# Kernel optimization log

Hardware: AMD Instinct MI355X
Metric: run time of the kernel (lower is better)

Reference implementation:

```python
import jax, jax.numpy as jnp
import numpy as np

N = 100000
E = 3200000
N_IN = 512
N_OUT = 256


def setup_inputs() -> dict:
    key = jax.random.key(0)
    k = jax.random.split(key, 6)
    stdv = 1.0 / np.sqrt(N_IN)
    x = jax.random.normal(k[0], (N, N_IN), dtype=jnp.float32)
    adj_rows = jax.random.randint(k[1], (E,), 0, N, dtype=jnp.int32)
    adj_cols = jax.random.randint(k[2], (E,), 0, N, dtype=jnp.int32)
    adj_vals = jax.random.uniform(k[3], (E,), dtype=jnp.float32)
    W = jax.random.uniform(k[4], (N_OUT, N_IN), minval=-stdv, maxval=stdv, dtype=jnp.float32)
    b = jax.random.uniform(k[5], (N_OUT,), minval=-stdv, maxval=stdv, dtype=jnp.float32)
    return {"x": x, "adj_rows": adj_rows, "adj_cols": adj_cols, "adj_vals": adj_vals, "W": W, "b": b}


def reference(x, adj_rows, adj_cols, adj_vals, W, b):
    # linear projection: x @ W^T + b  -> [N, n_out]
    h = jnp.einsum('ni,oi->no', x, W) + b
    # spmm: out[r] = sum_e adj_vals[e] * h[adj_cols[e]] for edges with row r
    msgs = h[adj_cols] * adj_vals[:, None]          # [E, n_out]
    out = jax.ops.segment_sum(msgs, adj_rows, num_segments=N)
    return out
```

## Files before the change

### kernel.cpp

```cpp
#include <hip/hip_runtime.h>

#define NIN 512
#define NOUT 256
#define NPART 8
#define RPB 32
#define BSH 5
#define CHUNK 2048
#define CSH 11
#define SEG 256
#define SEGSH 8
#define SCAT 1024

typedef __attribute__((ext_vector_type(8))) __bf16 bf16x8;
typedef __attribute__((ext_vector_type(4))) float f32x4;
typedef __attribute__((ext_vector_type(2))) int i32x2;

__device__ __forceinline__ ushort f2bf(float f) {
  uint u = __builtin_bit_cast(uint, f);
  uint r = (u + 0x7FFFu + ((u >> 16) & 1u)) >> 16;
  return (ushort)r;
}
__device__ __forceinline__ uint pk2(float a, float b) {
  return (uint)f2bf(a) | ((uint)f2bf(b) << 16);
}
__device__ __forceinline__ float bf2f(ushort u) {
  return __builtin_bit_cast(float, (uint)u << 16);
}

__global__ __launch_bounds__(256) void init_cur_kernel(int* __restrict__ cur,
                                                       int NB) {
  int i = blockIdx.x * 256 + threadIdx.x;
  if (i < NPART * NB) {
    int s = i / NB;
    int b = i - s * NB;
    cur[i] = ((b << 3) + s) << SEGSH;
  }
}

__global__ __launch_bounds__(512) void gemm_scatter_kernel(
    const float* __restrict__ x, const float* __restrict__ W,
    const float* __restrict__ bias, ushort* __restrict__ h, int M,
    const int* __restrict__ rows, const int* __restrict__ cols,
    const float* __restrict__ vals, int* __restrict__ cur,
    int2* __restrict__ bufE, int E, int NB, int nchunks, int G) {
  __shared__ ushort a_lds[128 * 40];
  __shared__ ushort b_lds[256 * 40];

  const int t = threadIdx.x;

  if (blockIdx.x >= G) {
    const int s = blockIdx.x & (NPART - 1);
    const int j = (int)blockIdx.x - G;
    const int m = j >> 3;
    const int nres = SCAT >> 3;
    int* mycur = cur + s * NB;
    for (int k = m;; k += nres) {
      int c = k * NPART + s;
      if (c >= nchunks) break;
      int i0 = c << CSH;
      int i1 = min(E, i0 + CHUNK);
      for (int i = i0 + t; i < i1; i += 512) {
        int r = __builtin_nontemporal_load(&rows[i]);
        int cc = __builtin_nontemporal_load(&cols[i]);
        float vv = __builtin_nontemporal_load(&vals[i]);
        int pos = atomicAdd(&mycur[r >> BSH], 1);
        int2 p;
        p.x = ((r & (RPB - 1)) << 17) | cc;
        p.y = __builtin_bit_cast(int, vv);
        bufE[pos] = p;
      }
    }
    return;
  }

  const int l = t & 63;
  const int wv = t >> 6;
  const int wr = wv >> 2;
  const int wc = wv & 3;
  const int m0 = blockIdx.x * 128;

  const int lrow = l & 15;
  const int lk = (l >> 4) * 8;

  f32x4 acc[4][4];
#pragma unroll
  for (int i = 0; i < 4; ++i)
#pragma unroll
    for (int j = 0; j < 4; ++j) acc[i][j] = (f32x4){0.f, 0.f, 0.f, 0.f};

  float biasr[4];
#pragma unroll
  for (int j = 0; j < 4; ++j) biasr[j] = bias[wc * 64 + j * 16 + lrow];

  const int arow = t >> 2;
  const int akc = (t & 3) * 8;
  const int brow = t >> 1;
  const int bkc = (t & 1) * 16;

  for (int k0 = 0; k0 < NIN; k0 += 32) {
    {
      float4 v0 = make_float4(0.f, 0.f, 0.f, 0.f), v1 = v0;
      if (m0 + arow < M) {
        const float4* xs =
            reinterpret_cast<const float4*>(x + (size_t)(m0 + arow) * NIN + k0 + akc);
        v0 = xs[0];
        v1 = xs[1];
      }
      uint4 p;
      p.x = pk2(v0.x, v0.y); p.y = pk2(v0.z, v0.w);
      p.z = pk2(v1.x, v1.y); p.w = pk2(v1.z, v1.w);
      *reinterpret_cast<uint4*>(&a_lds[arow * 40 + akc]) = p;
    }
    {
      const float4* wsrc =
          reinterpret_cast<const float4*>(W + (size_t)brow * NIN + k0 + bkc);
      float4 w0 = wsrc[0], w1 = wsrc[1], w2 = wsrc[2], w3 = wsrc[3];
      uint4 p0, p1;
      p0.x = pk2(w0.x, w0.y); p0.y = pk2(w0.z, w0.w);
      p0.z = pk2(w1.x, w1.y); p0.w = pk2(w1.z, w1.w);
      p1.x = pk2(w2.x, w2.y); p1.y = pk2(w2.z, w2.w);
      p1.z = pk2(w3.x, w3.y); p1.w = pk2(w3.z, w3.w);
      *reinterpret_cast<uint4*>(&b_lds[brow * 40 + bkc]) = p0;
      *reinterpret_cast<uint4*>(&b_lds[brow * 40 + bkc + 8]) = p1;
    }
    __syncthreads();

    bf16x8 af[4], bf_[4];
#pragma unroll
    for (int i = 0; i < 4; ++i)
      af[i] = *reinterpret_cast<const bf16x8*>(
          &a_lds[(wr * 64 + i * 16 + lrow) * 40 + lk]);
#pragma unroll
    for (int j = 0; j < 4; ++j)
      bf_[j] = *reinterpret_cast<const bf16x8*>(
          &b_lds[(wc * 64 + j * 16 + lrow) * 40 + lk]);
#pragma unroll
    for (int i = 0; i < 4; ++i)
#pragma unroll
      for (int j = 0; j < 4; ++j)
        acc[i][j] = __builtin_amdgcn_mfma_f32_16x16x32_bf16(af[i], bf_[j],
                                                            acc[i][j], 0, 0, 0);
    __syncthreads();
  }

#pragma unroll
  for (int i = 0; i < 4; ++i) {
    const int mbase = m0 + wr * 64 + i * 16 + (l >> 4) * 4;
#pragma unroll
    for (int r = 0; r < 4; ++r) {
      int m = mbase + r;
      if (m >= M) continue;
#pragma unroll
      for (int j = 0; j < 4; ++j)
        h[(size_t)m * NOUT + wc * 64 + j * 16 + lrow] =
            f2bf(acc[i][j][r] + biasr[j]);
    }
  }
}

__global__ __launch_bounds__(256) void bucket_reduce_kernel(
    const ushort* __restrict__ h, const int2* __restrict__ bufE,
    const int* __restrict__ cur, float* __restrict__ out, int M, int NB) {
  __shared__ int2 sbuf[NPART * SEG];
  __shared__ int cnt[RPB];
  __shared__ int off[RPB + 1];
  __shared__ int segn[NPART];

  const int b = blockIdx.x;
  const int t = threadIdx.x;

  if (t < NPART)
    segn[t] = min(cur[t * NB + b] - (((b << 3) + t) << SEGSH), SEG);
  if (t < RPB) cnt[t] = 0;
  __syncthreads();

  int2 ed[NPART];
#pragma unroll
  for (int s = 0; s < NPART; ++s) {
    int2 p = make_int2(0, 0);
    if (t < segn[s]) {
      i32x2 raw = __builtin_nontemporal_load(reinterpret_cast<const i32x2*>(
          &bufE[(size_t)(((b << 3) + s) << SEGSH) + t]));
      p.x = raw.x;
      p.y = raw.y;
      atomicAdd(&cnt[(uint)p.x >> 17], 1);
    }
    ed[s] = p;
  }
  __syncthreads();
  if (t == 0) {
    int run = 0;
#pragma unroll
    for (int j = 0; j < RPB; ++j) { off[j] = run; run += cnt[j]; }
    off[RPB] = run;
  }
  __syncthreads();
  if (t < RPB) cnt[t] = off[t];
  __syncthreads();
#pragma unroll
  for (int s = 0; s < NPART; ++s) {
    if (t < segn[s]) {
      int pos = atomicAdd(&cnt[(uint)ed[s].x >> 17], 1);
      sbuf[pos] = ed[s];
    }
  }
  __syncthreads();

  const int wv = t >> 6;
  const int lane = t & 63;
  for (int q = 0; q < 8; ++q) {
    int j = wv * 8 + q;
    int row = b * RPB + j;
    if (row >= M) break;
    int e = off[j];
    const int e1 = off[j + 1];
    f32x4 acc = (f32x4){0.f, 0.f, 0.f, 0.f};
    for (; e + 7 < e1; e += 8) {
      ushort4 hv[8];
      float vv[8];
#pragma unroll
      for (int u = 0; u < 8; ++u) {
        int2 p = sbuf[e + u];
        vv[u] = __builtin_bit_cast(float, p.y);
        hv[u] = *reinterpret_cast<const ushort4*>(
            h + (size_t)(p.x & 0x1FFFF) * NOUT + lane * 4);
      }
#pragma unroll
      for (int u = 0; u < 8; ++u) {
        acc.x += vv[u] * bf2f(hv[u].x);
        acc.y += vv[u] * bf2f(hv[u].y);
        acc.z += vv[u] * bf2f(hv[u].z);
        acc.w += vv[u] * bf2f(hv[u].w);
      }
    }
    for (; e < e1; ++e) {
      int2 p0 = sbuf[e];
      float v0 = __builtin_bit_cast(float, p0.y);
      ushort4 h0 = *reinterpret_cast<const ushort4*>(
          h + (size_t)(p0.x & 0x1FFFF) * NOUT + lane * 4);
      acc.x += v0 * bf2f(h0.x); acc.y += v0 * bf2f(h0.y);
      acc.z += v0 * bf2f(h0.z); acc.w += v0 * bf2f(h0.w);
    }
    __builtin_nontemporal_store(
        acc, reinterpret_cast<f32x4*>(out + (size_t)row * NOUT + lane * 4));
  }
}

extern "C" void kernel_launch(void* const* d_in, const int* in_sizes, int n_in,
                              void* d_out, int out_size, void* d_ws, size_t ws_size,
                              hipStream_t stream) {
  const float* x        = (const float*)d_in[0];
  const int*   adj_rows = (const int*)d_in[1];
  const int*   adj_cols = (const int*)d_in[2];
  const float* adj_vals = (const float*)d_in[3];
  const float* W        = (const float*)d_in[4];
  const float* b        = (const float*)d_in[5];
  float* out = (float*)d_out;

  const int M = in_sizes[0] / NIN;
  const int E = in_sizes[1];

  const int NB = (M + RPB - 1) >> BSH;
  const int nchunks = (E + CHUNK - 1) >> CSH;

  ushort* h    = (ushort*)d_ws;
  int2*   bufE = (int2*)(h + (size_t)M * NOUT);
  int*    cur  = (int*)(bufE + (size_t)NB * NPART * SEG);

  const int G = (M + 127) / 128;

  init_cur_kernel<<<(NPART * NB + 255) / 256, 256, 0, stream>>>(cur, NB);
  gemm_scatter_kernel<<<G + SCAT, 512, 0, stream>>>(
      x, W, b, h, M, adj_rows, adj_cols, adj_vals, cur, bufE, E, NB, nchunks, G);
  bucket_reduce_kernel<<<NB, 256, 0, stream>>>(h, bufE, cur, out, M, NB);
}
```

Before: 420.6 us.

## Split wavefront halves across edges with 16-byte gathers; prefetch next x tile in GEMM

The reduce kernel now has each half-wavefront handle a different edge, with each lane gathering 8 bf16 values (16 bytes) instead of 4. The two halves' partial sums are then combined with a shuffle before the store. This widens the per-lane gather and processes two edges per instruction, at the cost of extra shuffles and an odd-edge tail path. The GEMM also loads the next k-slice of x into registers before the MFMA work so global latency overlaps compute, at the cost of extra registers.

New measurement: 420.9 us. About the same (+0.1%).

```diff
diff --git a/kernel.cpp b/kernel.cpp
--- a/kernel.cpp
+++ b/kernel.cpp
@@ -13,7 +13,9 @@
 
 typedef __attribute__((ext_vector_type(8))) __bf16 bf16x8;
 typedef __attribute__((ext_vector_type(4))) float f32x4;
+typedef __attribute__((ext_vector_type(8))) float f32x8;
 typedef __attribute__((ext_vector_type(2))) int i32x2;
+typedef __attribute__((ext_vector_type(8))) ushort u16x8;
 
 __device__ __forceinline__ ushort f2bf(float f) {
   uint u = __builtin_bit_cast(uint, f);
@@ -97,18 +99,22 @@
   const int brow = t >> 1;
   const int bkc = (t & 1) * 16;
 
-  for (int k0 = 0; k0 < NIN; k0 += 32) {
+  const bool avalid = (m0 + arow < M);
+  const float* xbase = x + (size_t)(m0 + arow) * NIN + akc;
+
+  float4 xa = make_float4(0.f, 0.f, 0.f, 0.f), xb = xa;
+  if (avalid) {
+    const float4* xs = reinterpret_cast<const float4*>(xbase);
+    xa = xs[0];
+    xb = xs[1];
+  }
+
+  for (int kk = 0; kk < 16; ++kk) {
+    const int k0 = kk * 32;
     {
-      float4 v0 = make_float4(0.f, 0.f, 0.f, 0.f), v1 = v0;
-      if (m0 + arow < M) {
-        const float4* xs =
-            reinterpret_cast<const float4*>(x + (size_t)(m0 + arow) * NIN + k0 + akc);
-        v0 = xs[0];
-        v1 = xs[1];
-      }
       uint4 p;
-      p.x = pk2(v0.x, v0.y); p.y = pk2(v0.z, v0.w);
-      p.z = pk2(v1.x, v1.y); p.w = pk2(v1.z, v1.w);
+      p.x = pk2(xa.x, xa.y); p.y = pk2(xa.z, xa.w);
+      p.z = pk2(xb.x, xb.y); p.w = pk2(xb.z, xb.w);
       *reinterpret_cast<uint4*>(&a_lds[arow * 40 + akc]) = p;
     }
     {
@@ -125,6 +131,13 @@
     }
     __syncthreads();
 
+    float4 nxa = make_float4(0.f, 0.f, 0.f, 0.f), nxb = nxa;
+    if (kk < 15 && avalid) {
+      const float4* xs = reinterpret_cast<const float4*>(xbase + k0 + 32);
+      nxa = xs[0];
+      nxb = xs[1];
+    }
+
     bf16x8 af[4], bf_[4];
 #pragma unroll
     for (int i = 0; i < 4; ++i)
@@ -141,6 +154,8 @@
         acc[i][j] = __builtin_amdgcn_mfma_f32_16x16x32_bf16(af[i], bf_[j],
                                                             acc[i][j], 0, 0, 0);
     __syncthreads();
+    xa = nxa;
+    xb = nxb;
   }
 
 #pragma unroll
@@ -208,41 +223,55 @@
 
   const int wv = t >> 6;
   const int lane = t & 63;
+  const int half = lane >> 5;
+  const int hl = lane & 31;
   for (int q = 0; q < 8; ++q) {
     int j = wv * 8 + q;
     int row = b * RPB + j;
     if (row >= M) break;
     int e = off[j];
     const int e1 = off[j + 1];
-    f32x4 acc = (f32x4){0.f, 0.f, 0.f, 0.f};
+    f32x8 acc = (f32x8){0.f, 0.f, 0.f, 0.f, 0.f, 0.f, 0.f, 0.f};
     for (; e + 7 < e1; e += 8) {
-      ushort4 hv[8];
-      float vv[8];
-#pragma unroll
-      for (int u = 0; u < 8; ++u) {
-        int2 p = sbuf[e + u];
+      u16x8 hv[4];
+      float vv[4];
+#pragma unroll
+      for (int u = 0; u < 4; ++u) {
+        int2 p = sbuf[e + 2 * u + half];
         vv[u] = __builtin_bit_cast(float, p.y);
-        hv[u] = *reinterpret_cast<const ushort4*>(
-            h + (size_t)(p.x & 0x1FFFF) * NOUT + lane * 4);
+        hv[u] = *reinterpret_cast<const u16x8*>(
+            h + (size_t)(p.x & 0x1FFFF) * NOUT + hl * 8);
       }
 #pragma unroll
-      for (int u = 0; u < 8; ++u) {
-        acc.x += vv[u] * bf2f(hv[u].x);
-        acc.y += vv[u] * bf2f(hv[u].y);
-        acc.z += vv[u] * bf2f(hv[u].z);
-        acc.w += vv[u] * bf2f(hv[u].w);
-      }
-    }
-    for (; e < e1; ++e) {
-      int2 p0 = sbuf[e];
-      float v0 = __builtin_bit_cast(float, p0.y);
-      ushort4 h0 = *reinterpret_cast<const ushort4*>(
-          h + (size_t)(p0.x & 0x1FFFF) * NOUT + lane * 4);
-      acc.x += v0 * bf2f(h0.x); acc.y += v0 * bf2f(h0.y);
-      acc.z += v0 * bf2f(h0.z); acc.w += v0 * bf2f(h0.w);
-    }
-    __builtin_nontemporal_store(
-        acc, reinterpret_cast<f32x4*>(out + (size_t)row * NOUT + lane * 4));
+      for (int u = 0; u < 4; ++u)
+#pragma unroll
+        for (int c = 0; c < 8; ++c) acc[c] += vv[u] * bf2f(hv[u][c]);
+    }
+    for (; e + 1 < e1; e += 2) {
+      int2 p = sbuf[e + half];
+      float v = __builtin_bit_cast(float, p.y);
+      u16x8 hv = *reinterpret_cast<const u16x8*>(
+          h + (size_t)(p.x & 0x1FFFF) * NOUT + hl * 8);
+#pragma unroll
+      for (int c = 0; c < 8; ++c) acc[c] += v * bf2f(hv[c]);
+    }
+    if (e < e1) {
+      int2 p = sbuf[e];
+      float v = half ? 0.f : __builtin_bit_cast(float, p.y);
+      u16x8 hv = *reinterpret_cast<const u16x8*>(
+          h + (size_t)(p.x & 0x1FFFF) * NOUT + hl * 8);
+#pragma unroll
+      for (int c = 0; c < 8; ++c) acc[c] += v * bf2f(hv[c]);
+    }
+#pragma unroll
+    for (int c = 0; c < 8; ++c) acc[c] += __shfl(acc[c], hl + 32);
+    if (half == 0) {
+      f32x4 lo = (f32x4){acc[0], acc[1], acc[2], acc[3]};
+      f32x4 hi = (f32x4){acc[4], acc[5], acc[6], acc[7]};
+      f32x4* dst = reinterpret_cast<f32x4*>(out + (size_t)row * NOUT + hl * 8);
+      __builtin_nontemporal_store(lo, dst);
+      __builtin_nontemporal_store(hi, dst + 1);
+    }
   }
 }
 
```
